# Kernel tuning notes

Measured on AMD Instinct MI355X. Metric: run time of the kernel, lower is better.

The kernel has to match this reference:

```python
import jax, jax.numpy as jnp
import numpy as np

BLOCK_SIZE = 64
HIDDEN = 1024
INTERMEDIATE = 4096
NUM_BLOCK = HIDDEN // BLOCK_SIZE              # 16
INT_BLOCK = (INTERMEDIATE // HIDDEN) * BLOCK_SIZE  # 256


def setup_inputs() -> dict:
    key = jax.random.key(0)
    k_x, k_w1, k_b1, k_w2, k_b2 = jax.random.split(key, 5)
    hidden_states = jax.random.normal(k_x, (4, 2048, HIDDEN), dtype=jnp.float32)
    w1 = 0.02 * jax.random.normal(k_w1, (NUM_BLOCK, INT_BLOCK, BLOCK_SIZE), dtype=jnp.float32)
    b1 = 0.001 * jax.random.normal(k_b1, (INTERMEDIATE,), dtype=jnp.float32)
    w2 = 0.02 * jax.random.normal(k_w2, (NUM_BLOCK, BLOCK_SIZE, INT_BLOCK), dtype=jnp.float32)
    b2 = 0.001 * jax.random.normal(k_b2, (HIDDEN,), dtype=jnp.float32)
    return {"hidden_states": hidden_states, "w1": w1, "b1": b1, "w2": w2, "b2": b2}


def reference(hidden_states, w1, b1, w2, b2):
    lead = hidden_states.shape[:-1]
    dim = hidden_states.shape[-1]
    nb, ibs, bs = w1.shape  # num_block, intermediate_block_size, block_size
    x = hidden_states.reshape(-1, nb, bs)                 # [B, n, i]
    h = jnp.einsum('bni,noi->bno', x, w1)                 # [B, n, o]
    # channel shuffle: transpose block and feature axes before flattening
    h = jnp.swapaxes(h, -1, -2).reshape(-1, nb * ibs)     # [B, o*n order]
    h = jax.nn.gelu(h + b1, approximate=False)
    h = h.reshape(-1, nb, ibs)                            # regroup after shuffle
    y = jnp.einsum('bni,noi->bno', h, w2).reshape(-1, nb * bs) + b2
    return y.reshape(*lead, dim)
```

## Files before the change

### kernel.cpp

```cpp
#include <hip/hip_runtime.h>
#include <hip/hip_bf16.h>


typedef __attribute__((ext_vector_type(8))) short  short8;
typedef __attribute__((ext_vector_type(4))) short  short4v;
typedef __attribute__((ext_vector_type(4))) float  floatx4;

__device__ __forceinline__ short f2bf(float f) {
  union { __hip_bfloat16 h; short s; } u;
  u.h = __float2bfloat16(f);
  return u.s;
}
__device__ __forceinline__ float bf2f(short s) {
  union { float f; unsigned u; } uu;
  uu.u = ((unsigned)(unsigned short)s) << 16;
  return uu.f;
}

__device__ __forceinline__ float gelu_f(float v) {
  float m = v * v;
  float c = fmaf(-0.1029375f, m, -2.3020807f);
  float z = v * c;
  float e = __builtin_amdgcn_exp2f(z);
  return v * __builtin_amdgcn_rcpf(1.0f + e);
}

__global__ void pack_k(const float* __restrict__ w1, const float* __restrict__ w2,
                       const float* __restrict__ b1, short* __restrict__ w1p,
                       short* __restrict__ w2p, short* __restrict__ b1p) {
  const int t = blockIdx.x * blockDim.x + threadIdx.x;
  const int lane = t & 63;
  const int lhi = lane >> 4;
  if (t < 32768) {
    const int ks = (t >> 6) & 1, np = (t >> 7) & 15, n = (t >> 11) & 15;
    const float* src = w1 + ((size_t)(n * 256 + np * 16 + (lane & 15)) * 64 + ks * 32 + lhi * 8);
    short8 f;
#pragma unroll
    for (int e = 0; e < 8; ++e) f[e] = f2bf(src[e]);
    *(short8*)(w1p + (size_t)t * 8) = f;
  } else if (t < 65536) {
    const int t2 = t - 32768;
    const int ot = (t2 >> 6) & 3, ks = (t2 >> 8) & 7, np = (t2 >> 11) & 15;
    const int op = ot * 16 + (lane & 15);
    short8 f;
#pragma unroll
    for (int e = 0; e < 8; ++e) {
      const int k = ks * 32 + lhi * 8 + e;
      f[e] = f2bf(w2[(size_t)(np * 64 + op) * 256 + (k & 15) * 16 + (k >> 4)]);
    }
    *(short8*)(w2p + (size_t)t2 * 8) = f;
  } else {
    const int t3 = t - 65536;
    const int np = (t3 >> 6) & 15, n = (t3 >> 10) & 15;
    short4v b;
#pragma unroll
    for (int r = 0; r < 4; ++r) b[r] = f2bf(b1[(np * 16 + lhi * 4 + r) * 16 + n]);
    *(short4v*)(b1p + (size_t)((n * 16 + np) * 64 + lane) * 4) = b;
  }
}

__global__ __launch_bounds__(256, 4) void fused_k(
    const float* __restrict__ x, const short* __restrict__ w1p,
    const short* __restrict__ w2p, const short* __restrict__ b1p,
    const float* __restrict__ b2, float* __restrict__ y) {
  __shared__ __align__(16) short xs[16 * 1024];
  __shared__ __align__(16) short ch[4 * 16 * 64];

  const int tid = threadIdx.x;
  const int wv = tid >> 6, lane = tid & 63;
  const int l15 = lane & 15, lhi = lane >> 4;
  const int rt  = blockIdx.x >> 1;
  const int nph = blockIdx.x & 1;

#pragma unroll
  for (int p = 0; p < 4; ++p) {
    const int row = wv * 4 + p;
    const int rsw = (row & 7) << 3;
#pragma unroll
    for (int q = 0; q < 4; ++q) {
      const int col = q * 256 + lane * 4;
      floatx4 v = *(const floatx4*)(x + (size_t)(rt * 16 + row) * 1024 + col);
      short4v s;
#pragma unroll
      for (int e = 0; e < 4; ++e) s[e] = f2bf(v[e]);
      *(short4v*)(&xs[row * 1024 + (col ^ rsw)]) = s;
    }
  }
  __syncthreads();

  const int swz = (l15 & 7) << 3;
  short* myc = ch + wv * 1024;

#pragma unroll
  for (int it = 0; it < 2; ++it) {
    const int np = nph * 8 + wv * 2 + it;
    floatx4 acc2[4] = {{0.f,0.f,0.f,0.f},{0.f,0.f,0.f,0.f},
                       {0.f,0.f,0.f,0.f},{0.f,0.f,0.f,0.f}};

#pragma unroll
    for (int h = 0; h < 4; ++h) {
#pragma unroll
      for (int nn = 0; nn < 4; ++nn) {
        const int n = h * 4 + nn;
        short8 xf0 = *(const short8*)(&xs[l15 * 1024 + ((n * 64 + lhi * 8) ^ swz)]);
        short8 xf1 = *(const short8*)(&xs[l15 * 1024 + ((n * 64 + 32 + lhi * 8) ^ swz)]);
        short8 wf0 = *(const short8*)(w1p + (size_t)(((n * 16 + np) * 2 + 0) * 64 + lane) * 8);
        short8 wf1 = *(const short8*)(w1p + (size_t)(((n * 16 + np) * 2 + 1) * 64 + lane) * 8);
        short4v bv = *(const short4v*)(b1p + (size_t)((n * 16 + np) * 64 + lane) * 4);
        floatx4 acc = {0.f, 0.f, 0.f, 0.f};
        acc = __builtin_amdgcn_mfma_f32_16x16x32_bf16(wf0, xf0, acc, 0, 0, 0);
        acc = __builtin_amdgcn_mfma_f32_16x16x32_bf16(wf1, xf1, acc, 0, 0, 0);
        short4v hv;
#pragma unroll
        for (int e = 0; e < 4; ++e)
          hv[e] = f2bf(gelu_f(acc[e] + bf2f(bv[e])));
        *(short4v*)(&myc[l15 * 64 + ((nn * 16 + lhi * 4) ^ swz)]) = hv;
      }
      short8 af0 = *(const short8*)(&myc[l15 * 64 + ((0 * 32 + lhi * 8) ^ swz)]);
      short8 af1 = *(const short8*)(&myc[l15 * 64 + ((1 * 32 + lhi * 8) ^ swz)]);
#pragma unroll
      for (int ot = 0; ot < 4; ++ot) {
        short8 bf0 = *(const short8*)(w2p + (size_t)(((np * 8 + 2 * h) * 4 + ot) * 64 + lane) * 8);
        short8 bf1 = *(const short8*)(w2p + (size_t)(((np * 8 + 2 * h + 1) * 4 + ot) * 64 + lane) * 8);
        acc2[ot] = __builtin_amdgcn_mfma_f32_16x16x32_bf16(af0, bf0, acc2[ot], 0, 0, 0);
        acc2[ot] = __builtin_amdgcn_mfma_f32_16x16x32_bf16(af1, bf1, acc2[ot], 0, 0, 0);
      }
    }

#pragma unroll
    for (int ot = 0; ot < 4; ++ot) {
      const int col = np * 64 + ot * 16 + l15;
      const float bb = b2[col];
      float* py = y + (size_t)(rt * 16 + lhi * 4) * 1024 + col;
#pragma unroll
      for (int r = 0; r < 4; ++r)
        py[(size_t)r * 1024] = acc2[ot][r] + bb;
    }
  }
}

extern "C" void kernel_launch(void* const* d_in, const int* in_sizes, int n_in,
                              void* d_out, int out_size, void* d_ws, size_t ws_size,
                              hipStream_t stream) {
  const float* x  = (const float*)d_in[0];
  const float* w1 = (const float*)d_in[1];
  const float* b1 = (const float*)d_in[2];
  const float* w2 = (const float*)d_in[3];
  const float* b2 = (const float*)d_in[4];
  float* y = (float*)d_out;

  short* w1p = (short*)d_ws;
  short* w2p = w1p + 16 * 256 * 64;
  short* b1p = w2p + 16 * 256 * 64;

  pack_k<<<160, 512, 0, stream>>>(w1, w2, b1, w1p, w2p, b1p);
  fused_k<<<1024, 256, 0, stream>>>(x, w1p, w2p, b1p, b2, y);
}
```

Before: 48.28 us.

## Feed GELU outputs straight into second MFMA via register permutation of W2 packing

The W2 packing order is permuted so that the first MFMA's output layout matches the A-operand layout of the second MFMA. GELU results can then be packed in registers and fed directly into the second matmul, which removes the per-wave LDS staging buffer and its write/read round trip. The grid is doubled so each wave handles one output block, and the x tile uses row padding instead of an XOR swizzle. The trade-off is that each block now reloads the x tile for fewer output blocks, doubling the x global reads and bf16 conversion work.

```diff
diff --git a/kernel.cpp b/kernel.cpp
--- a/kernel.cpp
+++ b/kernel.cpp
@@ -5,6 +5,8 @@
 typedef __attribute__((ext_vector_type(8))) short  short8;
 typedef __attribute__((ext_vector_type(4))) short  short4v;
 typedef __attribute__((ext_vector_type(4))) float  floatx4;
+
+#define XP 1032
 
 __device__ __forceinline__ short f2bf(float f) {
   union { __hip_bfloat16 h; short s; } u;
@@ -15,6 +17,9 @@
   union { float f; unsigned u; } uu;
   uu.u = ((unsigned)(unsigned short)s) << 16;
   return uu.f;
+}
+__device__ __forceinline__ int pk16(float a, float b) {
+  return (int)(unsigned short)f2bf(a) | ((int)(unsigned short)f2bf(b) << 16);
 }
 
 __device__ __forceinline__ float gelu_f(float v) {
@@ -40,13 +45,14 @@
     *(short8*)(w1p + (size_t)t * 8) = f;
   } else if (t < 65536) {
     const int t2 = t - 32768;
-    const int ot = (t2 >> 6) & 3, ks = (t2 >> 8) & 7, np = (t2 >> 11) & 15;
+    const int ot = (t2 >> 6) & 3, s = (t2 >> 8) & 7, np = (t2 >> 11) & 15;
     const int op = ot * 16 + (lane & 15);
     short8 f;
 #pragma unroll
     for (int e = 0; e < 8; ++e) {
-      const int k = ks * 32 + lhi * 8 + e;
-      f[e] = f2bf(w2[(size_t)(np * 64 + op) * 256 + (k & 15) * 16 + (k >> 4)]);
+      const int Kc = 32 * s + 16 * ((e >> 2) & 1) + 4 * lhi + (e & 3);
+      const int n = Kc >> 4, ohi = Kc & 15;
+      f[e] = f2bf(w2[(size_t)(np * 64 + op) * 256 + ohi * 16 + n]);
     }
     *(short8*)(w2p + (size_t)t2 * 8) = f;
   } else {
@@ -63,79 +69,93 @@
     const float* __restrict__ x, const short* __restrict__ w1p,
     const short* __restrict__ w2p, const short* __restrict__ b1p,
     const float* __restrict__ b2, float* __restrict__ y) {
-  __shared__ __align__(16) short xs[16 * 1024];
-  __shared__ __align__(16) short ch[4 * 16 * 64];
+  __shared__ __align__(16) short xs[16 * XP];
 
   const int tid = threadIdx.x;
   const int wv = tid >> 6, lane = tid & 63;
   const int l15 = lane & 15, lhi = lane >> 4;
-  const int rt  = blockIdx.x >> 1;
-  const int nph = blockIdx.x & 1;
+  const int rt  = blockIdx.x >> 2;
+  const int np  = (blockIdx.x & 3) * 4 + wv;
 
 #pragma unroll
   for (int p = 0; p < 4; ++p) {
     const int row = wv * 4 + p;
-    const int rsw = (row & 7) << 3;
 #pragma unroll
     for (int q = 0; q < 4; ++q) {
       const int col = q * 256 + lane * 4;
       floatx4 v = *(const floatx4*)(x + (size_t)(rt * 16 + row) * 1024 + col);
-      short4v s;
+      short4v sv;
 #pragma unroll
-      for (int e = 0; e < 4; ++e) s[e] = f2bf(v[e]);
-      *(short4v*)(&xs[row * 1024 + (col ^ rsw)]) = s;
+      for (int e = 0; e < 4; ++e) sv[e] = f2bf(v[e]);
+      *(short4v*)(&xs[row * XP + col]) = sv;
     }
   }
   __syncthreads();
 
-  const int swz = (l15 & 7) << 3;
-  short* myc = ch + wv * 1024;
+  floatx4 c0 = {0.f,0.f,0.f,0.f}, c1 = {0.f,0.f,0.f,0.f};
+  floatx4 c2 = {0.f,0.f,0.f,0.f}, c3 = {0.f,0.f,0.f,0.f};
 
 #pragma unroll
-  for (int it = 0; it < 2; ++it) {
-    const int np = nph * 8 + wv * 2 + it;
-    floatx4 acc2[4] = {{0.f,0.f,0.f,0.f},{0.f,0.f,0.f,0.f},
-                       {0.f,0.f,0.f,0.f},{0.f,0.f,0.f,0.f}};
+  for (int s = 0; s < 8; ++s) {
+    int pka0, pka1, pkb0, pkb1;
 
-#pragma unroll
-    for (int h = 0; h < 4; ++h) {
-#pragma unroll
-      for (int nn = 0; nn < 4; ++nn) {
-        const int n = h * 4 + nn;
-        short8 xf0 = *(const short8*)(&xs[l15 * 1024 + ((n * 64 + lhi * 8) ^ swz)]);
-        short8 xf1 = *(const short8*)(&xs[l15 * 1024 + ((n * 64 + 32 + lhi * 8) ^ swz)]);
-        short8 wf0 = *(const short8*)(w1p + (size_t)(((n * 16 + np) * 2 + 0) * 64 + lane) * 8);
-        short8 wf1 = *(const short8*)(w1p + (size_t)(((n * 16 + np) * 2 + 1) * 64 + lane) * 8);
-        short4v bv = *(const short4v*)(b1p + (size_t)((n * 16 + np) * 64 + lane) * 4);
-        floatx4 acc = {0.f, 0.f, 0.f, 0.f};
-        acc = __builtin_amdgcn_mfma_f32_16x16x32_bf16(wf0, xf0, acc, 0, 0, 0);
-        acc = __builtin_amdgcn_mfma_f32_16x16x32_bf16(wf1, xf1, acc, 0, 0, 0);
-        short4v hv;
-#pragma unroll
-        for (int e = 0; e < 4; ++e)
-          hv[e] = f2bf(gelu_f(acc[e] + bf2f(bv[e])));
-        *(short4v*)(&myc[l15 * 64 + ((nn * 16 + lhi * 4) ^ swz)]) = hv;
-      }
-      short8 af0 = *(const short8*)(&myc[l15 * 64 + ((0 * 32 + lhi * 8) ^ swz)]);
-      short8 af1 = *(const short8*)(&myc[l15 * 64 + ((1 * 32 + lhi * 8) ^ swz)]);
-#pragma unroll
-      for (int ot = 0; ot < 4; ++ot) {
-        short8 bf0 = *(const short8*)(w2p + (size_t)(((np * 8 + 2 * h) * 4 + ot) * 64 + lane) * 8);
-        short8 bf1 = *(const short8*)(w2p + (size_t)(((np * 8 + 2 * h + 1) * 4 + ot) * 64 + lane) * 8);
-        acc2[ot] = __builtin_amdgcn_mfma_f32_16x16x32_bf16(af0, bf0, acc2[ot], 0, 0, 0);
-        acc2[ot] = __builtin_amdgcn_mfma_f32_16x16x32_bf16(af1, bf1, acc2[ot], 0, 0, 0);
-      }
+    {
+      const int n = 2 * s;
+      short8 xf0 = *(const short8*)(&xs[l15 * XP + n * 64 + lhi * 8]);
+      short8 xf1 = *(const short8*)(&xs[l15 * XP + n * 64 + 32 + lhi * 8]);
+      short8 wf0 = *(const short8*)(w1p + (size_t)(((n * 16 + np) * 2 + 0) * 64 + lane) * 8);
+      short8 wf1 = *(const short8*)(w1p + (size_t)(((n * 16 + np) * 2 + 1) * 64 + lane) * 8);
+      short4v bv = *(const short4v*)(b1p + (size_t)((n * 16 + np) * 64 + lane) * 4);
+      floatx4 acc = {0.f, 0.f, 0.f, 0.f};
+      acc = __builtin_amdgcn_mfma_f32_16x16x32_bf16(wf0, xf0, acc, 0, 0, 0);
+      acc = __builtin_amdgcn_mfma_f32_16x16x32_bf16(wf1, xf1, acc, 0, 0, 0);
+      const float g0 = gelu_f(acc[0] + bf2f(bv[0]));
+      const float g1 = gelu_f(acc[1] + bf2f(bv[1]));
+      const float g2 = gelu_f(acc[2] + bf2f(bv[2]));
+      const float g3 = gelu_f(acc[3] + bf2f(bv[3]));
+      pka0 = pk16(g0, g1);
+      pka1 = pk16(g2, g3);
+    }
+    {
+      const int n = 2 * s + 1;
+      short8 xf0 = *(const short8*)(&xs[l15 * XP + n * 64 + lhi * 8]);
+      short8 xf1 = *(const short8*)(&xs[l15 * XP + n * 64 + 32 + lhi * 8]);
+      short8 wf0 = *(const short8*)(w1p + (size_t)(((n * 16 + np) * 2 + 0) * 64 + lane) * 8);
+      short8 wf1 = *(const short8*)(w1p + (size_t)(((n * 16 + np) * 2 + 1) * 64 + lane) * 8);
+      short4v bv = *(const short4v*)(b1p + (size_t)((n * 16 + np) * 64 + lane) * 4);
+      floatx4 acc = {0.f, 0.f, 0.f, 0.f};
+      acc = __builtin_amdgcn_mfma_f32_16x16x32_bf16(wf0, xf0, acc, 0, 0, 0);
+      acc = __builtin_amdgcn_mfma_f32_16x16x32_bf16(wf1, xf1, acc, 0, 0, 0);
+      const float g0 = gelu_f(acc[0] + bf2f(bv[0]));
+      const float g1 = gelu_f(acc[1] + bf2f(bv[1]));
+      const float g2 = gelu_f(acc[2] + bf2f(bv[2]));
+      const float g3 = gelu_f(acc[3] + bf2f(bv[3]));
+      pkb0 = pk16(g0, g1);
+      pkb1 = pk16(g2, g3);
     }
 
+    union { int i[4]; short8 v; } af;
+    af.i[0] = pka0; af.i[1] = pka1; af.i[2] = pkb0; af.i[3] = pkb1;
+    const size_t wb = (size_t)((np * 8 + s) * 4) * 64 * 8;
+    short8 bf0 = *(const short8*)(w2p + wb + (size_t)(0 * 64 + lane) * 8);
+    short8 bf1 = *(const short8*)(w2p + wb + (size_t)(1 * 64 + lane) * 8);
+    short8 bf2v = *(const short8*)(w2p + wb + (size_t)(2 * 64 + lane) * 8);
+    short8 bf3 = *(const short8*)(w2p + wb + (size_t)(3 * 64 + lane) * 8);
+    c0 = __builtin_amdgcn_mfma_f32_16x16x32_bf16(af.v, bf0, c0, 0, 0, 0);
+    c1 = __builtin_amdgcn_mfma_f32_16x16x32_bf16(af.v, bf1, c1, 0, 0, 0);
+    c2 = __builtin_amdgcn_mfma_f32_16x16x32_bf16(af.v, bf2v, c2, 0, 0, 0);
+    c3 = __builtin_amdgcn_mfma_f32_16x16x32_bf16(af.v, bf3, c3, 0, 0, 0);
+  }
+
+  floatx4 cc[4] = {c0, c1, c2, c3};
 #pragma unroll
-    for (int ot = 0; ot < 4; ++ot) {
-      const int col = np * 64 + ot * 16 + l15;
-      const float bb = b2[col];
-      float* py = y + (size_t)(rt * 16 + lhi * 4) * 1024 + col;
+  for (int ot = 0; ot < 4; ++ot) {
+    const int col = np * 64 + ot * 16 + l15;
+    const float bb = b2[col];
+    float* py = y + (size_t)(rt * 16 + lhi * 4) * 1024 + col;
 #pragma unroll
-      for (int r = 0; r < 4; ++r)
-        py[(size_t)r * 1024] = acc2[ot][r] + bb;
-    }
+    for (int r = 0; r < 4; ++r)
+      py[(size_t)r * 1024] = cc[ot][r] + bb;
   }
 }
 
@@ -154,5 +174,5 @@
   short* b1p = w2p + 16 * 256 * 64;
 
   pack_k<<<160, 512, 0, stream>>>(w1, w2, b1, w1p, w2p, b1p);
-  fused_k<<<1024, 256, 0, stream>>>(x, w1p, w2p, b1p, b2, y);
+  fused_k<<<2048, 256, 0, stream>>>(x, w1p, w2p, b1p, b2, y);
 }
```

Result: no change. 47.49 us (-1.6%).
